# Kernel optimization log

Hardware: AMD Instinct MI355X
Metric: run time of the kernel (lower is better)

Reference implementation:

```python
import jax, jax.numpy as jnp
import numpy as np
import math

N, L, D = 1024, 32, 768
N_OUT, IN_DIM, OUT_DIM = 16, 64, 64
EPS = 1e-8


def setup_inputs() -> dict:
    key = jax.random.key(0)
    ks = jax.random.split(key, 4)
    x = jax.random.normal(ks[0], (N, L, D), jnp.float32)
    mask = jnp.ones((N, L), jnp.float32)
    scaled = lambda k, shape, fan: jax.random.normal(k, shape, jnp.float32) * (1.0 / np.sqrt(fan).astype(np.float32))
    Wscore = scaled(ks[1], (L, D, 1), D)
    Bscore = jnp.zeros((L, 1, 1), jnp.float32)
    Wcap = scaled(ks[2], (L, D, IN_DIM), D)
    Bcap = jnp.zeros((L, 1, IN_DIM), jnp.float32)
    Wvote = scaled(ks[3], (L, N_OUT, IN_DIM, OUT_DIM), IN_DIM)
    Bvote = jnp.zeros((L, N_OUT, 1, OUT_DIM), jnp.float32)
    beta_use = jnp.zeros((L, 1, 1, 1), jnp.float32)
    beta_ign = jnp.zeros((1, N_OUT, 1, 1), jnp.float32)
    return dict(x=x, mask=mask, Wscore=Wscore, Bscore=Bscore, Wcap=Wcap,
                Bcap=Bcap, Wvote=Wvote, Bvote=Bvote, beta_use=beta_use,
                beta_ign=beta_ign, iters=3)


def reference(x, mask, Wscore, Bscore, Wcap, Bcap, Wvote, Bvote, beta_use, beta_ign, iters):
    n_out = Wvote.shape[1]
    half_pi = np.float32(0.5 * math.pi)
    x_t = jnp.transpose(x, (1, 0, 2))                      # [L, N, D]
    a_in = jnp.matmul(x_t, Wscore) + Bscore                # [L, N, 1]
    mu_in = jax.nn.gelu(jnp.matmul(x_t, Wcap) + Bcap, approximate=False)  # [L, N, in_dim]
    f_a_in = jax.nn.sigmoid(a_in) * jnp.transpose(mask)[..., None]        # [L, N, 1]
    f_a_in = f_a_in[:, None, :, :]                         # [L, 1, N, 1]
    # votes: [L, n_out, N, out_dim] (einsum avoids materializing repeated mu_in)
    V = jnp.einsum('lni,lkio->lkno', mu_in, Wvote) + Bvote

    R = jnp.full((1, n_out, 1, 1), 1.0 / n_out, dtype=x.dtype)
    a_out = mu_out = var_out = None
    for t in range(iters):
        if t > 0:
            log_p = (-jnp.sum((V - mu_out[None]) ** 2 / (2.0 * var_out[None] + EPS), axis=-1)
                     - 1.0 - half_pi
                     - 0.5 * jnp.sum(jnp.log(var_out[None] + EPS), axis=-1))   # [L, n_out, N]
            R = jax.nn.softmax(jax.nn.log_sigmoid(a_out)[None] + log_p[..., None], axis=1)
        D_use = f_a_in * R                                  # [L, n_out, N, 1]
        D_ign = f_a_in - D_use
        a_out = jnp.sum(beta_use * D_use, axis=0) - jnp.sum(beta_ign * D_ign, axis=0)  # [n_out, N, 1]
        denom = jnp.sum(D_use, axis=0) + EPS                # [n_out, N, 1]
        mu_out = jnp.sum(D_use * V, axis=0) / denom         # [n_out, N, out_dim]
        var_out = jnp.sum(D_use * (V - mu_out[None]) ** 2, axis=0) / denom

    a_fin = jnp.transpose(a_out[..., 0])                    # [N, n_out]
    mu_fin = jnp.transpose(mu_out, (1, 0, 2))               # [N, n_out, out_dim]
    return a_fin, mu_fin
```

## Files before the change

kernel.cpp:

```cpp
#include <hip/hip_runtime.h>
#include <hip/hip_bf16.h>

#define L_DIM 32
#define N_DIM 1024
#define D_DIM 768
#define K_DIM 16
#define I_DIM 64
#define O_DIM 64
#define EPSF 1e-8f
#define PX 72

typedef unsigned short u16;
typedef __attribute__((ext_vector_type(8))) short short8;
typedef __attribute__((ext_vector_type(4))) float f32x4;
#define MFMA __builtin_amdgcn_mfma_f32_16x16x32_bf16

__device__ __forceinline__ float bf2f(u16 v) {
    union { unsigned int u; float f; } x; x.u = ((unsigned int)v) << 16; return x.f;
}
__device__ __forceinline__ u16 f2bf(float f) {
    union { float f; unsigned int u; } x; x.f = f;
    unsigned int u = x.u;
    u += 0x7FFFu + ((u >> 16) & 1u);
    return (u16)(u >> 16);
}
__device__ __forceinline__ void split2(float v, u16& h, u16& l) {
    u16 hh = f2bf(v);
    h = hh;
    l = f2bf(v - bf2f(hh));
}
__device__ __forceinline__ void store_split4(u16* ph, u16* pl, float4 v) {
    unsigned u0 = __float_as_uint(v.x), u1 = __float_as_uint(v.y);
    unsigned u2 = __float_as_uint(v.z), u3 = __float_as_uint(v.w);
    uint2 H, L;
    H.x = (u0 >> 16) | (u1 & 0xFFFF0000u);
    H.y = (u2 >> 16) | (u3 & 0xFFFF0000u);
    float l0 = v.x - __uint_as_float(u0 & 0xFFFF0000u);
    float l1 = v.y - __uint_as_float(u1 & 0xFFFF0000u);
    float l2 = v.z - __uint_as_float(u2 & 0xFFFF0000u);
    float l3 = v.w - __uint_as_float(u3 & 0xFFFF0000u);
    L.x = (__float_as_uint(l0) >> 16) | (__float_as_uint(l1) & 0xFFFF0000u);
    L.y = (__float_as_uint(l2) >> 16) | (__float_as_uint(l3) & 0xFFFF0000u);
    *(uint2*)ph = H;
    *(uint2*)pl = L;
}

__global__ __launch_bounds__(256) void prep_w(
    const float* __restrict__ Wc, u16* __restrict__ cH, u16* __restrict__ cL,
    const float* __restrict__ Wv, u16* __restrict__ vH, u16* __restrict__ vL)
{
    const int l = blockIdx.y, t = threadIdx.x;
    __shared__ float tile[64][65];
    if (blockIdx.x < 12) {
        const int d0 = blockIdx.x * 64;
        #pragma unroll
        for (int p = 0; p < 4; p++) {
            int dd = p * 16 + (t >> 4), i4 = (t & 15) * 4;
            float4 v = *(const float4*)&Wc[((size_t)l * D_DIM + d0 + dd) * I_DIM + i4];
            tile[dd][i4] = v.x; tile[dd][i4+1] = v.y; tile[dd][i4+2] = v.z; tile[dd][i4+3] = v.w;
        }
        __syncthreads();
        #pragma unroll
        for (int p = 0; p < 4; p++) {
            int i = p * 16 + (t >> 4), dd0 = (t & 15) * 4;
            u16 h[4], lo[4];
            #pragma unroll
            for (int j = 0; j < 4; j++) split2(tile[dd0 + j][i], h[j], lo[j]);
            size_t base = ((size_t)l * I_DIM + i) * D_DIM + d0 + dd0;
            uint2 ph; ph.x = h[0] | ((unsigned)h[1] << 16); ph.y = h[2] | ((unsigned)h[3] << 16);
            uint2 pl; pl.x = lo[0] | ((unsigned)lo[1] << 16); pl.y = lo[2] | ((unsigned)lo[3] << 16);
            *(uint2*)&cH[base] = ph;
            *(uint2*)&cL[base] = pl;
        }
    } else {
        const int k = blockIdx.x - 12;
        #pragma unroll
        for (int p = 0; p < 4; p++) {
            int i = p * 16 + (t >> 4), o4 = (t & 15) * 4;
            float4 v = *(const float4*)&Wv[(((size_t)l * K_DIM + k) * I_DIM + i) * O_DIM + o4];
            tile[i][o4] = v.x; tile[i][o4+1] = v.y; tile[i][o4+2] = v.z; tile[i][o4+3] = v.w;
        }
        __syncthreads();
        #pragma unroll
        for (int p = 0; p < 4; p++) {
            int o = p * 16 + (t >> 4), i0 = (t & 15) * 4;
            u16 h[4], lo[4];
            #pragma unroll
            for (int j = 0; j < 4; j++) split2(tile[i0 + j][o], h[j], lo[j]);
            size_t base = (((size_t)l * K_DIM + k) * O_DIM + o) * I_DIM + i0;
            uint2 ph; ph.x = h[0] | ((unsigned)h[1] << 16); ph.y = h[2] | ((unsigned)h[3] << 16);
            uint2 pl; pl.x = lo[0] | ((unsigned)lo[1] << 16); pl.y = lo[2] | ((unsigned)lo[3] << 16);
            *(uint2*)&vH[base] = ph;
            *(uint2*)&vL[base] = pl;
        }
    }
}

#define A_CHUNK(K0, R0, R1, WH0, WL0, WH1, WL1, BUF)                        \
  {                                                                          \
    const float* wp = &wsc_s[(K0) + sd];                                     \
    fa0 += R0.x * wp[0] + R0.y * wp[1] + R0.z * wp[2] + R0.w * wp[3];        \
    fa1 += R1.x * wp[0] + R1.y * wp[1] + R1.z * wp[2] + R1.w * wp[3];        \
    store_split4(&xh[BUF][sg][sd],      &xl[BUF][sg][sd],      R0);          \
    store_split4(&xh[BUF][16 + sg][sd], &xl[BUF][16 + sg][sd], R1);          \
    __syncthreads();                                                         \
    if ((K0) + 128 < D_DIM) {                                                \
      R0 = *(const float4*)&x[xoff0 + (K0) + 128 + sd];                      \
      R1 = *(const float4*)&x[xoff1 + (K0) + 128 + sd];                      \
    }                                                                        \
    {                                                                        \
      short8 bh, bl;                                                         \
      bh = *(const short8*)&xh[BUF][ln16][quad * 8];                         \
      bl = *(const short8*)&xl[BUF][ln16][quad * 8];                         \
      acc0 = MFMA(WH0, bh, acc0, 0, 0, 0);                                   \
      acc0 = MFMA(WH0, bl, acc0, 0, 0, 0);                                   \
      acc0 = MFMA(WL0, bh, acc0, 0, 0, 0);                                   \
      bh = *(const short8*)&xh[BUF][16 + ln16][quad * 8];                    \
      bl = *(const short8*)&xl[BUF][16 + ln16][quad * 8];                    \
      acc1 = MFMA(WH0, bh, acc1, 0, 0, 0);                                   \
      acc1 = MFMA(WH0, bl, acc1, 0, 0, 0);                                   \
      acc1 = MFMA(WL0, bh, acc1, 0, 0, 0);                                   \
      bh = *(const short8*)&xh[BUF][ln16][32 + quad * 8];                    \
      bl = *(const short8*)&xl[BUF][ln16][32 + quad * 8];                    \
      acc0 = MFMA(WH1, bh, acc0, 0, 0, 0);                                   \
      acc0 = MFMA(WH1, bl, acc0, 0, 0, 0);                                   \
      acc0 = MFMA(WL1, bh, acc0, 0, 0, 0);                                   \
      bh = *(const short8*)&xh[BUF][16 + ln16][32 + quad * 8];               \
      bl = *(const short8*)&xl[BUF][16 + ln16][32 + quad * 8];               \
      acc1 = MFMA(WH1, bh, acc1, 0, 0, 0);                                   \
      acc1 = MFMA(WH1, bl, acc1, 0, 0, 0);                                   \
      acc1 = MFMA(WL1, bh, acc1, 0, 0, 0);                                   \
    }                                                                        \
    if ((K0) + 128 < D_DIM) {                                                \
      WH0 = *(const short8*)&WcH[wrow + (K0) + 128];                         \
      WL0 = *(const short8*)&WcL[wrow + (K0) + 128];                         \
      WH1 = *(const short8*)&WcH[wrow + (K0) + 160];                         \
      WL1 = *(const short8*)&WcL[wrow + (K0) + 160];                         \
    }                                                                        \
  }

__global__ __launch_bounds__(256, 4) void kernelA(
    const float* __restrict__ x, const float* __restrict__ mask,
    const float* __restrict__ Wscore, const float* __restrict__ Bscore,
    const u16* __restrict__ WcH, const u16* __restrict__ WcL,
    const float* __restrict__ Bcap,
    float* __restrict__ mu_out, float* __restrict__ fa_out,
    int nbase, int nchunk)
{
    const int bid  = blockIdx.y * gridDim.x + blockIdx.x;
    const int slot = bid >> 3;
    const int l    = (bid & 7) + 8 * (slot & 3);
    const int n0l  = (slot >> 2) * 32;

    const int t    = threadIdx.x;
    const int w    = t >> 6;
    const int lane = t & 63;
    const int quad = lane >> 4;
    const int ln16 = lane & 15;

    __shared__ u16 xh[2][32][PX], xl[2][32][PX];
    __shared__ float wsc_s[D_DIM];
    __shared__ float bcap_s[64];

    for (int i = t; i < D_DIM; i += 256) wsc_s[i] = Wscore[l * D_DIM + i];
    if (t < 64) bcap_s[t] = Bcap[l * I_DIM + t];

    const int sg = t >> 4;
    const int sd = (t & 15) * 4;

    const size_t xoff0 = ((size_t)(nbase + n0l + sg) * L_DIM + l) * D_DIM;
    const size_t xoff1 = ((size_t)(nbase + n0l + 16 + sg) * L_DIM + l) * D_DIM;

    float4 r0a = *(const float4*)&x[xoff0 + sd];
    float4 r1a = *(const float4*)&x[xoff1 + sd];
    float4 r0b = *(const float4*)&x[xoff0 + 64 + sd];
    float4 r1b = *(const float4*)&x[xoff1 + 64 + sd];

    const size_t wrow = ((size_t)l * I_DIM + (w * 16 + ln16)) * D_DIM + quad * 8;
    short8 wha0 = *(const short8*)&WcH[wrow];
    short8 wla0 = *(const short8*)&WcL[wrow];
    short8 wha1 = *(const short8*)&WcH[wrow + 32];
    short8 wla1 = *(const short8*)&WcL[wrow + 32];
    short8 whb0 = *(const short8*)&WcH[wrow + 64];
    short8 wlb0 = *(const short8*)&WcL[wrow + 64];
    short8 whb1 = *(const short8*)&WcH[wrow + 96];
    short8 wlb1 = *(const short8*)&WcL[wrow + 96];

    __syncthreads();

    f32x4 acc0 = {0.f, 0.f, 0.f, 0.f};
    f32x4 acc1 = {0.f, 0.f, 0.f, 0.f};
    float fa0 = 0.f, fa1 = 0.f;

    #pragma unroll
    for (int cc = 0; cc < 6; cc++) {
        A_CHUNK(cc * 128,      r0a, r1a, wha0, wla0, wha1, wla1, 0)
        A_CHUNK(cc * 128 + 64, r0b, r1b, whb0, wlb0, whb1, wlb1, 1)
    }

    fa0 += __shfl_xor(fa0, 1, 64); fa1 += __shfl_xor(fa1, 1, 64);
    fa0 += __shfl_xor(fa0, 2, 64); fa1 += __shfl_xor(fa1, 2, 64);
    fa0 += __shfl_xor(fa0, 4, 64); fa1 += __shfl_xor(fa1, 4, 64);
    fa0 += __shfl_xor(fa0, 8, 64); fa1 += __shfl_xor(fa1, 8, 64);
    if ((t & 15) == 0) {
        float bs = Bscore[l];
        {
            float a = fa0 + bs;
            float sig = 1.f / (1.f + expf(-a));
            float m = mask[(size_t)(nbase + n0l + sg) * L_DIM + l];
            fa_out[(size_t)l * nchunk + n0l + sg] = sig * m;
        }
        {
            float a = fa1 + bs;
            float sig = 1.f / (1.f + expf(-a));
            float m = mask[(size_t)(nbase + n0l + 16 + sg) * L_DIM + l];
            fa_out[(size_t)l * nchunk + n0l + 16 + sg] = sig * m;
        }
    }

    #pragma unroll
    for (int c = 0; c < 2; c++) {
        const f32x4 a = (c == 0) ? acc0 : acc1;
        const int n = c * 16 + ln16;
        const int i0 = w * 16 + quad * 4;
        float4 o;
        float* op = (float*)&o;
        #pragma unroll
        for (int r = 0; r < 4; r++) {
            float v = a[r] + bcap_s[i0 + r];
            op[r] = 0.5f * v * (1.f + erff(v * 0.70710678118f));
        }
        *(float4*)&mu_out[((size_t)l * nchunk + n0l + n) * I_DIM + i0] = o;
    }
}

__global__ __launch_bounds__(256) void kernelB(
    const float* __restrict__ mu_in,
    const u16* __restrict__ WvH, const u16* __restrict__ WvL,
    const float* __restrict__ Bvote,
    float* __restrict__ V, int nchunk)
{
    const int bid  = (blockIdx.z * gridDim.y + blockIdx.y) * gridDim.x + blockIdx.x;
    const int slot = bid >> 3;
    const int l    = (bid & 7) + 8 * (slot & 3);
    const int rem  = slot >> 2;
    const int k    = rem & 15;
    const int n0l  = (rem >> 4) * 64;

    const int t    = threadIdx.x;
    const int w    = t >> 6;
    const int lane = t & 63;
    const int quad = lane >> 4;
    const int ln16 = lane & 15;

    __shared__ u16 mh[64][PX], ml[64][PX];
    __shared__ float bvote_s[64];

    const int srow = t >> 4, scol = (t & 15) * 4;
    float4 m0 = *(const float4*)&mu_in[((size_t)l * nchunk + n0l + srow) * I_DIM + scol];
    float4 m1 = *(const float4*)&mu_in[((size_t)l * nchunk + n0l + 16 + srow) * I_DIM + scol];
    float4 m2 = *(const float4*)&mu_in[((size_t)l * nchunk + n0l + 32 + srow) * I_DIM + scol];
    float4 m3 = *(const float4*)&mu_in[((size_t)l * nchunk + n0l + 48 + srow) * I_DIM + scol];

    const size_t wrow = (((size_t)l * K_DIM + k) * O_DIM + (w * 16 + ln16)) * I_DIM + quad * 8;
    short8 ah0 = *(const short8*)&WvH[wrow];
    short8 al0 = *(const short8*)&WvL[wrow];
    short8 ah1 = *(const short8*)&WvH[wrow + 32];
    short8 al1 = *(const short8*)&WvL[wrow + 32];

    if (t < 64) bvote_s[t] = Bvote[((size_t)l * K_DIM + k) * O_DIM + t];

    store_split4(&mh[srow][scol],      &ml[srow][scol],      m0);
    store_split4(&mh[16 + srow][scol], &ml[16 + srow][scol], m1);
    store_split4(&mh[32 + srow][scol], &ml[32 + srow][scol], m2);
    store_split4(&mh[48 + srow][scol], &ml[48 + srow][scol], m3);
    __syncthreads();

    f32x4 acc[4] = {{0.f,0.f,0.f,0.f},{0.f,0.f,0.f,0.f},{0.f,0.f,0.f,0.f},{0.f,0.f,0.f,0.f}};

    #pragma unroll
    for (int c = 0; c < 4; c++) {
        const int n = c * 16 + ln16;
        short8 bh = *(const short8*)&mh[n][quad * 8];
        short8 bl = *(const short8*)&ml[n][quad * 8];
        acc[c] = MFMA(ah0, bh, acc[c], 0, 0, 0);
        acc[c] = MFMA(ah0, bl, acc[c], 0, 0, 0);
        acc[c] = MFMA(al0, bh, acc[c], 0, 0, 0);
    }
    #pragma unroll
    for (int c = 0; c < 4; c++) {
        const int n = c * 16 + ln16;
        short8 bh = *(const short8*)&mh[n][32 + quad * 8];
        short8 bl = *(const short8*)&ml[n][32 + quad * 8];
        acc[c] = MFMA(ah1, bh, acc[c], 0, 0, 0);
        acc[c] = MFMA(ah1, bl, acc[c], 0, 0, 0);
        acc[c] = MFMA(al1, bh, acc[c], 0, 0, 0);
    }

    #pragma unroll
    for (int c = 0; c < 4; c++) {
        const int n = c * 16 + ln16;
        const int o0 = w * 16 + quad * 4;
        float4 o;
        o.x = acc[c][0] + bvote_s[o0];
        o.y = acc[c][1] + bvote_s[o0 + 1];
        o.z = acc[c][2] + bvote_s[o0 + 2];
        o.w = acc[c][3] + bvote_s[o0 + 3];
        *(float4*)&V[(((size_t)l * K_DIM + k) * nchunk + n0l + n) * O_DIM + o0] = o;
    }
}

__global__ __launch_bounds__(512, 4) void kernelC(
    const float* __restrict__ V, const float* __restrict__ fa_in,
    const float* __restrict__ beta_use, const float* __restrict__ beta_ign,
    const int* __restrict__ iters_p,
    float* __restrict__ out, int nbase, int nchunk)
{
    const int nl   = blockIdx.x;
    const int ng   = nbase + nl;
    const int t    = threadIdx.x;
    const int k    = t >> 5;
    const int op   = t & 31;
    const int o0   = op * 2;
    const int lane = t & 63;
    int iters = iters_p[0];
    if (iters < 0 || iters > 16) iters = 3;

    __shared__ float fa_s[32];
    __shared__ float bu_s[32];
    __shared__ float R_s[32][17];
    __shared__ float sc_s[32][17];

    if (t < 32) {
        fa_s[t] = fa_in[(size_t)t * nchunk + nl];
        bu_s[t] = beta_use[t];
    }
    R_s[t >> 4][t & 15] = 1.f / 16.f;
    const float bi_k = beta_ign[k];

    float2 Vr[32];
    #pragma unroll
    for (int l = 0; l < 32; l++)
        Vr[l] = *(const float2*)&V[(((size_t)l * K_DIM + k) * nchunk + nl) * O_DIM + o0];
    __syncthreads();

    float mu0 = 0.f, mu1 = 0.f, var0 = 0.f, var1 = 0.f, a_r = 0.f;

    for (int it = 0; it < iters; it++) {
        if (it > 0) {
            float g0 = 1.f / (2.f * var0 + EPSF);
            float g1 = 1.f / (2.f * var1 + EPSF);
            float lvp = logf(var0 + EPSF) + logf(var1 + EPSF);
            lvp += __shfl_xor(lvp, 1, 64);
            lvp += __shfl_xor(lvp, 2, 64);
            lvp += __shfl_xor(lvp, 4, 64);
            lvp += __shfl_xor(lvp, 8, 64);
            lvp += __shfl_xor(lvp, 16, 64);
            float ls = fminf(a_r, 0.f) - log1pf(expf(-fabsf(a_r)));
            const float cst = ls - 1.f - 1.57079632679f - 0.5f * lvp;

            const bool s16 = (lane & 16) != 0;
            const bool s8  = (lane & 8)  != 0;
            const bool s4  = (lane & 4)  != 0;
            const bool s2  = (lane & 2)  != 0;
            const bool s1  = (lane & 1)  != 0;
            float w16[16];
            #pragma unroll
            for (int j = 0; j < 16; j++) {
                float d0 = Vr[j].x - mu0,      d1 = Vr[j].y - mu1;
                float a  = d0 * d0 * g0 + d1 * d1 * g1;
                float e0 = Vr[j + 16].x - mu0, e1 = Vr[j + 16].y - mu1;
                float b  = e0 * e0 * g0 + e1 * e1 * g1;
                float ta = a + __shfl_xor(a, 16, 64);
                float tb = b + __shfl_xor(b, 16, 64);
                w16[j] = s16 ? tb : ta;
            }
            float w8[8];
            #pragma unroll
            for (int j = 0; j < 8; j++) {
                float ta = w16[j]     + __shfl_xor(w16[j],     8, 64);
                float tb = w16[j + 8] + __shfl_xor(w16[j + 8], 8, 64);
                w8[j] = s8 ? tb : ta;
            }
            float w4[4];
            #pragma unroll
            for (int j = 0; j < 4; j++) {
                float ta = w8[j]     + __shfl_xor(w8[j],     4, 64);
                float tb = w8[j + 4] + __shfl_xor(w8[j + 4], 4, 64);
                w4[j] = s4 ? tb : ta;
            }
            float w2[2];
            #pragma unroll
            for (int j = 0; j < 2; j++) {
                float ta = w2[0];
                (void)ta;
                float taa = w4[j]     + __shfl_xor(w4[j],     2, 64);
                float tbb = w4[j + 2] + __shfl_xor(w4[j + 2], 2, 64);
                w2[j] = s2 ? tbb : taa;
            }
            float ta2 = w2[0] + __shfl_xor(w2[0], 1, 64);
            float tb2 = w2[1] + __shfl_xor(w2[1], 1, 64);
            float w1 = s1 ? tb2 : ta2;
            sc_s[lane & 31][k] = cst - w1;
            __syncthreads();

            {
                const int lr = t >> 4;
                const int kk = t & 15;
                float s0 = sc_s[lr][kk];
                float m = s0;
                m = fmaxf(m, __shfl_xor(m, 1, 64));
                m = fmaxf(m, __shfl_xor(m, 2, 64));
                m = fmaxf(m, __shfl_xor(m, 4, 64));
                m = fmaxf(m, __shfl_xor(m, 8, 64));
                float e = expf(s0 - m);
                float sum = e;
                sum += __shfl_xor(sum, 1, 64);
                sum += __shfl_xor(sum, 2, 64);
                sum += __shfl_xor(sum, 4, 64);
                sum += __shfl_xor(sum, 8, 64);
                R_s[lr][kk] = e / sum;
            }
            __syncthreads();
        }
        float denom = EPSF, a_acc = 0.f;
        float mua0 = 0.f, mua1 = 0.f, v2a0 = 0.f, v2a1 = 0.f;
        #pragma unroll
        for (int l = 0; l < 32; l++) {
            float Du = fa_s[l] * R_s[l][k];
            denom += Du;
            a_acc += bu_s[l] * Du - bi_k * (fa_s[l] - Du);
            float dv0 = Du * Vr[l].x;
            float dv1 = Du * Vr[l].y;
            mua0 += dv0;  v2a0 += dv0 * Vr[l].x;
            mua1 += dv1;  v2a1 += dv1 * Vr[l].y;
        }
        float invd = 1.f / denom;
        mu0 = mua0 * invd;
        mu1 = mua1 * invd;
        var0 = fmaxf(v2a0 * invd - mu0 * mu0, 0.f);
        var1 = fmaxf(v2a1 * invd - mu1 * mu1, 0.f);
        a_r = a_acc;
    }

    if (op == 0) out[(size_t)ng * K_DIM + k] = a_r;
    float2 o2; o2.x = mu0; o2.y = mu1;
    *(float2*)&out[(size_t)N_DIM * K_DIM + ((size_t)ng * K_DIM + k) * O_DIM + o0] = o2;
}

extern "C" void kernel_launch(void* const* d_in, const int* in_sizes, int n_in,
                              void* d_out, int out_size, void* d_ws, size_t ws_size,
                              hipStream_t stream) {
    (void)out_size;
    static const int EXP[11] = {25165824, 32768, 24576, 32, 1572864, 64,
                                2097152, 65536, 32, 16, 1};
    int mapi[11];
    bool used[64] = {false};
    for (int s = 0; s < 11; s++) {
        mapi[s] = (s < n_in) ? s : 0;
        for (int j = 0; j < n_in && j < 64; j++) {
            if (!used[j] && in_sizes[j] == EXP[s]) { mapi[s] = j; used[j] = true; break; }
        }
    }
    const float* x        = (const float*)d_in[mapi[0]];
    const float* mask     = (const float*)d_in[mapi[1]];
    const float* Wscore   = (const float*)d_in[mapi[2]];
    const float* Bscore   = (const float*)d_in[mapi[3]];
    const float* Wcap     = (const float*)d_in[mapi[4]];
    const float* Bcap     = (const float*)d_in[mapi[5]];
    const float* Wvote    = (const float*)d_in[mapi[6]];
    const float* Bvote    = (const float*)d_in[mapi[7]];
    const float* beta_use = (const float*)d_in[mapi[8]];
    const float* beta_ign = (const float*)d_in[mapi[9]];
    const int*   iters    = (const int*)d_in[mapi[10]];
    float* out = (float*)d_out;

    const size_t WCAP = (size_t)L_DIM * I_DIM * D_DIM;
    const size_t WVOT = (size_t)L_DIM * K_DIM * O_DIM * I_DIM;
    const size_t WBYTES = 2 * WCAP * 2 + 2 * WVOT * 2;

    int C = 64;
    {
        const int cands[5] = {1024, 512, 256, 128, 64};
        for (int i = 0; i < 5; i++) {
            size_t need = WBYTES + (size_t)cands[i] * (128 + 8192 + 131072);
            if (need <= ws_size) { C = cands[i]; break; }
        }
    }

    char* ws = (char*)d_ws;
    u16* WcH = (u16*)ws;
    u16* WcL = (u16*)(ws + WCAP * 2);
    u16* WvH = (u16*)(ws + WCAP * 4);
    u16* WvL = (u16*)(ws + WCAP * 4 + WVOT * 2);
    char* dyn = ws + WBYTES;
    float* fa = (float*)dyn;
    float* mu = (float*)(dyn + (size_t)128 * C);
    float* V  = (float*)(dyn + (size_t)128 * C + (size_t)8192 * C);

    prep_w<<<dim3(28, 32), 256, 0, stream>>>(Wcap, WcH, WcL, Wvote, WvH, WvL);

    for (int nbase = 0; nbase < N_DIM; nbase += C) {
        kernelA<<<dim3(C / 32, 32), 256, 0, stream>>>(
            x, mask, Wscore, Bscore, WcH, WcL, Bcap, mu, fa, nbase, C);
        kernelB<<<dim3(C / 64, 16, 32), 256, 0, stream>>>(
            mu, WvH, WvL, Bvote, V, C);
        kernelC<<<dim3(C), 512, 0, stream>>>(
            V, fa, beta_use, beta_ign, iters, out, nbase, C);
    }
}
```

Measured before the change: 265.5 us.

## Fuse capsule projection and vote GEMM into one kernel via shared-memory mu

Merges kernelA and kernelB so that the GELU'd capsule activations stay in shared memory as split bf16 hi/lo tiles, and the vote GEMM over all 16 output capsules runs in the same block, with Wvote fragments double-buffered across k. This drops the global mu round trip and one kernel launch per chunk, and reduces the workspace needed per chunk. In exchange each block does 16x more vote work serially, grid parallelism for the vote stage falls, and LDS use per block grows.

```diff
diff --git a/kernel.cpp b/kernel.cpp
--- a/kernel.cpp
+++ b/kernel.cpp
@@ -139,12 +139,65 @@
     }                                                                        \
   }
 
-__global__ __launch_bounds__(256, 4) void kernelA(
+#define V_STEP(KK, AH0, AL0, AH1, AL1, NH0, NL0, NH1, NL1, PRE)              \
+  {                                                                          \
+    if (PRE) {                                                               \
+      const size_t wn = wrowV + (size_t)((KK) + 1) * (O_DIM * I_DIM);        \
+      NH0 = *(const short8*)&WvH[wn];                                        \
+      NL0 = *(const short8*)&WvL[wn];                                        \
+      NH1 = *(const short8*)&WvH[wn + 32];                                   \
+      NL1 = *(const short8*)&WvL[wn + 32];                                   \
+    }                                                                        \
+    f32x4 vac0 = {0.f,0.f,0.f,0.f}, vac1 = {0.f,0.f,0.f,0.f};                \
+    {                                                                        \
+      short8 bh, bl;                                                         \
+      bh = *(const short8*)&muh[ln16][quad * 8];                             \
+      bl = *(const short8*)&mul[ln16][quad * 8];                             \
+      vac0 = MFMA(AH0, bh, vac0, 0, 0, 0);                                   \
+      vac0 = MFMA(AH0, bl, vac0, 0, 0, 0);                                   \
+      vac0 = MFMA(AL0, bh, vac0, 0, 0, 0);                                   \
+      bh = *(const short8*)&muh[16 + ln16][quad * 8];                        \
+      bl = *(const short8*)&mul[16 + ln16][quad * 8];                        \
+      vac1 = MFMA(AH0, bh, vac1, 0, 0, 0);                                   \
+      vac1 = MFMA(AH0, bl, vac1, 0, 0, 0);                                   \
+      vac1 = MFMA(AL0, bh, vac1, 0, 0, 0);                                   \
+      bh = *(const short8*)&muh[ln16][32 + quad * 8];                        \
+      bl = *(const short8*)&mul[ln16][32 + quad * 8];                        \
+      vac0 = MFMA(AH1, bh, vac0, 0, 0, 0);                                   \
+      vac0 = MFMA(AH1, bl, vac0, 0, 0, 0);                                   \
+      vac0 = MFMA(AL1, bh, vac0, 0, 0, 0);                                   \
+      bh = *(const short8*)&muh[16 + ln16][32 + quad * 8];                   \
+      bl = *(const short8*)&mul[16 + ln16][32 + quad * 8];                   \
+      vac1 = MFMA(AH1, bh, vac1, 0, 0, 0);                                   \
+      vac1 = MFMA(AH1, bl, vac1, 0, 0, 0);                                   \
+      vac1 = MFMA(AL1, bh, vac1, 0, 0, 0);                                   \
+    }                                                                        \
+    {                                                                        \
+      const int o0 = w * 16 + quad * 4;                                     \
+      float4 o;                                                              \
+      o.x = vac0[0] + bvote_s[KK][o0];                                       \
+      o.y = vac0[1] + bvote_s[KK][o0 + 1];                                   \
+      o.z = vac0[2] + bvote_s[KK][o0 + 2];                                   \
+      o.w = vac0[3] + bvote_s[KK][o0 + 3];                                   \
+      *(float4*)&V[(((size_t)l * K_DIM + (KK)) * nchunk + n0l + ln16)        \
+                   * O_DIM + o0] = o;                                        \
+      o.x = vac1[0] + bvote_s[KK][o0];                                       \
+      o.y = vac1[1] + bvote_s[KK][o0 + 1];                                   \
+      o.z = vac1[2] + bvote_s[KK][o0 + 2];                                   \
+      o.w = vac1[3] + bvote_s[KK][o0 + 3];                                   \
+      *(float4*)&V[(((size_t)l * K_DIM + (KK)) * nchunk + n0l + 16 + ln16)   \
+                   * O_DIM + o0] = o;                                        \
+    }                                                                        \
+  }
+
+__global__ __launch_bounds__(256, 4) void kernelAB(
     const float* __restrict__ x, const float* __restrict__ mask,
     const float* __restrict__ Wscore, const float* __restrict__ Bscore,
     const u16* __restrict__ WcH, const u16* __restrict__ WcL,
     const float* __restrict__ Bcap,
-    float* __restrict__ mu_out, float* __restrict__ fa_out,
+    const u16* __restrict__ WvH, const u16* __restrict__ WvL,
+    const float* __restrict__ Bvote,
+    float* __restrict__ V, float* __restrict__ fa_out,
     int nbase, int nchunk)
 {
     const int bid  = blockIdx.y * gridDim.x + blockIdx.x;
@@ -159,11 +212,19 @@
     const int ln16 = lane & 15;
 
     __shared__ u16 xh[2][32][PX], xl[2][32][PX];
+    __shared__ u16 muh[32][PX], mul[32][PX];
     __shared__ float wsc_s[D_DIM];
     __shared__ float bcap_s[64];
+    __shared__ float bvote_s[K_DIM][64];
 
     for (int i = t; i < D_DIM; i += 256) wsc_s[i] = Wscore[l * D_DIM + i];
     if (t < 64) bcap_s[t] = Bcap[l * I_DIM + t];
+    #pragma unroll
+    for (int j = 0; j < 4; j++) {
+        int idx = j * 256 + t;
+        bvote_s[idx >> 6][idx & 63] =
+            Bvote[((size_t)l * K_DIM + (idx >> 6)) * O_DIM + (idx & 63)];
+    }
 
     const int sg = t >> 4;
     const int sd = (t & 15) * 4;
@@ -230,83 +291,21 @@
             float v = a[r] + bcap_s[i0 + r];
             op[r] = 0.5f * v * (1.f + erff(v * 0.70710678118f));
         }
-        *(float4*)&mu_out[((size_t)l * nchunk + n0l + n) * I_DIM + i0] = o;
-    }
-}
-
-__global__ __launch_bounds__(256) void kernelB(
-    const float* __restrict__ mu_in,
-    const u16* __restrict__ WvH, const u16* __restrict__ WvL,
-    const float* __restrict__ Bvote,
-    float* __restrict__ V, int nchunk)
-{
-    const int bid  = (blockIdx.z * gridDim.y + blockIdx.y) * gridDim.x + blockIdx.x;
-    const int slot = bid >> 3;
-    const int l    = (bid & 7) + 8 * (slot & 3);
-    const int rem  = slot >> 2;
-    const int k    = rem & 15;
-    const int n0l  = (rem >> 4) * 64;
-
-    const int t    = threadIdx.x;
-    const int w    = t >> 6;
-    const int lane = t & 63;
-    const int quad = lane >> 4;
-    const int ln16 = lane & 15;
-
-    __shared__ u16 mh[64][PX], ml[64][PX];
-    __shared__ float bvote_s[64];
-
-    const int srow = t >> 4, scol = (t & 15) * 4;
-    float4 m0 = *(const float4*)&mu_in[((size_t)l * nchunk + n0l + srow) * I_DIM + scol];
-    float4 m1 = *(const float4*)&mu_in[((size_t)l * nchunk + n0l + 16 + srow) * I_DIM + scol];
-    float4 m2 = *(const float4*)&mu_in[((size_t)l * nchunk + n0l + 32 + srow) * I_DIM + scol];
-    float4 m3 = *(const float4*)&mu_in[((size_t)l * nchunk + n0l + 48 + srow) * I_DIM + scol];
-
-    const size_t wrow = (((size_t)l * K_DIM + k) * O_DIM + (w * 16 + ln16)) * I_DIM + quad * 8;
-    short8 ah0 = *(const short8*)&WvH[wrow];
-    short8 al0 = *(const short8*)&WvL[wrow];
-    short8 ah1 = *(const short8*)&WvH[wrow + 32];
-    short8 al1 = *(const short8*)&WvL[wrow + 32];
-
-    if (t < 64) bvote_s[t] = Bvote[((size_t)l * K_DIM + k) * O_DIM + t];
-
-    store_split4(&mh[srow][scol],      &ml[srow][scol],      m0);
-    store_split4(&mh[16 + srow][scol], &ml[16 + srow][scol], m1);
-    store_split4(&mh[32 + srow][scol], &ml[32 + srow][scol], m2);
-    store_split4(&mh[48 + srow][scol], &ml[48 + srow][scol], m3);
+        store_split4(&muh[n][i0], &mul[n][i0], o);
+    }
     __syncthreads();
 
-    f32x4 acc[4] = {{0.f,0.f,0.f,0.f},{0.f,0.f,0.f,0.f},{0.f,0.f,0.f,0.f},{0.f,0.f,0.f,0.f}};
+    const size_t wrowV = ((size_t)l * K_DIM * O_DIM + (w * 16 + ln16)) * I_DIM + quad * 8;
+    short8 vha0 = *(const short8*)&WvH[wrowV];
+    short8 vla0 = *(const short8*)&WvL[wrowV];
+    short8 vha1 = *(const short8*)&WvH[wrowV + 32];
+    short8 vla1 = *(const short8*)&WvL[wrowV + 32];
+    short8 vhb0, vlb0, vhb1, vlb1;
 
     #pragma unroll
-    for (int c = 0; c < 4; c++) {
-        const int n = c * 16 + ln16;
-        short8 bh = *(const short8*)&mh[n][quad * 8];
-        short8 bl = *(const short8*)&ml[n][quad * 8];
-        acc[c] = MFMA(ah0, bh, acc[c], 0, 0, 0);
-        acc[c] = MFMA(ah0, bl, acc[c], 0, 0, 0);
-        acc[c] = MFMA(al0, bh, acc[c], 0, 0, 0);
-    }
-    #pragma unroll
-    for (int c = 0; c < 4; c++) {
-        const int n = c * 16 + ln16;
-        short8 bh = *(const short8*)&mh[n][32 + quad * 8];
-        short8 bl = *(const short8*)&ml[n][32 + quad * 8];
-        acc[c] = MFMA(ah1, bh, acc[c], 0, 0, 0);
-        acc[c] = MFMA(ah1, bl, acc[c], 0, 0, 0);
-        acc[c] = MFMA(al1, bh, acc[c], 0, 0, 0);
-    }
-
-    #pragma unroll
-    for (int c = 0; c < 4; c++) {
-        const int n = c * 16 + ln16;
-        const int o0 = w * 16 + quad * 4;
-        float4 o;
-        o.x = acc[c][0] + bvote_s[o0];
-        o.y = acc[c][1] + bvote_s[o0 + 1];
-        o.z = acc[c][2] + bvote_s[o0 + 2];
-        o.w = acc[c][3] + bvote_s[o0 + 3];
-        *(float4*)&V[(((size_t)l * K_DIM + k) * nchunk + n0l + n) * O_DIM + o0] = o;
+    for (int kk = 0; kk < K_DIM; kk += 2) {
+        V_STEP(kk,     vha0, vla0, vha1, vla1, vhb0, vlb0, vhb1, vlb1, 1)
+        V_STEP(kk + 1, vhb0, vlb0, vhb1, vlb1, vha0, vla0, vha1, vla1, (kk + 2 < K_DIM))
     }
 }
 
@@ -392,8 +391,6 @@
             float w2[2];
             #pragma unroll
             for (int j = 0; j < 2; j++) {
-                float ta = w2[0];
-                (void)ta;
                 float taa = w4[j]     + __shfl_xor(w4[j],     2, 64);
                 float tbb = w4[j + 2] + __shfl_xor(w4[j + 2], 2, 64);
                 w2[j] = s2 ? tbb : taa;
@@ -483,7 +480,7 @@
     {
         const int cands[5] = {1024, 512, 256, 128, 64};
         for (int i = 0; i < 5; i++) {
-            size_t need = WBYTES + (size_t)cands[i] * (128 + 8192 + 131072);
+            size_t need = WBYTES + (size_t)cands[i] * (128 + 131072);
             if (need <= ws_size) { C = cands[i]; break; }
         }
     }
@@ -495,16 +492,14 @@
     u16* WvL = (u16*)(ws + WCAP * 4 + WVOT * 2);
     char* dyn = ws + WBYTES;
     float* fa = (float*)dyn;
-    float* mu = (float*)(dyn + (size_t)128 * C);
-    float* V  = (float*)(dyn + (size_t)128 * C + (size_t)8192 * C);
+    float* V  = (float*)(dyn + (size_t)128 * C);
 
     prep_w<<<dim3(28, 32), 256, 0, stream>>>(Wcap, WcH, WcL, Wvote, WvH, WvL);
 
     for (int nbase = 0; nbase < N_DIM; nbase += C) {
-        kernelA<<<dim3(C / 32, 32), 256, 0, stream>>>(
-            x, mask, Wscore, Bscore, WcH, WcL, Bcap, mu, fa, nbase, C);
-        kernelB<<<dim3(C / 64, 16, 32), 256, 0, stream>>>(
-            mu, WvH, WvL, Bvote, V, C);
+        kernelAB<<<dim3(C / 32, 32), 256, 0, stream>>>(
+            x, mask, Wscore, Bscore, WcH, WcL, Bcap,
+            WvH, WvL, Bvote, V, fa, nbase, C);
         kernelC<<<dim3(C), 512, 0, stream>>>(
             V, fa, beta_use, beta_ign, iters, out, nbase, C);
     }
```

After: 298.6 us. 12.5% more time.
